# Kernel optimization log

Hardware: AMD Instinct MI355X
Metric: run time of the kernel (lower is better)

## Reference

```python
import jax, jax.numpy as jnp
import numpy as np

N, D, F, E, TOP_K = 8192, 1024, 2048, 8, 2


def setup_inputs() -> dict:
    key = jax.random.key(0)
    ks = jax.random.split(key, 8)
    s = 0.02
    x = jax.random.normal(ks[0], (N, D), dtype=jnp.float32)
    Wr = jax.random.normal(ks[1], (D, E), dtype=jnp.float32) * s  # router
    br = jnp.zeros((E,), jnp.float32)
    W1 = jax.random.normal(ks[2], (E, D, F), dtype=jnp.float32) * s  # expert FFN in
    b1 = jnp.zeros((E, F), jnp.float32)
    W2 = jax.random.normal(ks[3], (E, F, D), dtype=jnp.float32) * s  # expert FFN out
    b2 = jnp.zeros((E, D), jnp. float32)
    return {"x": x, "Wr": Wr, "br": br, "W1": W1, "b1": b1, "W2": W2, "b2": b2}


def reference(x, Wr, br, W1, b1, W2, b2):
    # Router: per-token expert logits -> softmax probabilities -> top-k sampler.
    logits = x @ Wr + br                         # [N, E]
    probs = jax.nn.softmax(logits, axis=-1)      # [N, E]
    top_p, top_i = jax.lax.top_k(probs, TOP_K)   # [N, K]
    # Combine weights: prob mass only on the selected top-k experts per token.
    w = (jax.nn.one_hot(top_i, E, dtype=x.dtype) * top_p[..., None]).sum(axis=1)  # [N, E]
    # Per-expert gather-compute-scatter, expressed as masked full-batch expert FFN
    # (identical math: tokens not routed to expert e have weight 0).
    out = jnp.zeros((x.shape[0], W2.shape[-1]), dtype=x.dtype)
    for e in range(E):  # small fixed loop over structurally distinct experts
        h = jax.nn.gelu(x @ W1[e] + b1[e])       # [N, F]
        y = h @ W2[e] + b2[e]                    # [N, D]
        out = out + w[:, e:e + 1] * y            # weighted scatter-add combine
    return out
```

## Files before the change

kernel.cpp:

```cpp
#include <hip/hip_runtime.h>
#include <hip/hip_bf16.h>


#define N_TOK 8192
#define DIM   1024
#define FF    2048
#define NE    8

typedef unsigned short ushort_t;
typedef __bf16 bf16x8 __attribute__((ext_vector_type(8)));
typedef float  f32x4  __attribute__((ext_vector_type(4)));
typedef unsigned short u16x8 __attribute__((ext_vector_type(8)));

__device__ __forceinline__ ushort_t f2bf(float f) {
    union { float f; unsigned int u; } v; v.f = f;
    unsigned int r = (v.u + 0x7FFFu + ((v.u >> 16) & 1u)) >> 16;
    return (ushort_t)r;
}

__device__ __forceinline__ void gload_lds16(const ushort_t* g, ushort_t* l) {
    __builtin_amdgcn_global_load_lds(
        (const __attribute__((address_space(1))) void*)g,
        (__attribute__((address_space(3))) void*)l,
        16, 0, 0);
}

__global__ __launch_bounds__(256) void transpose_conv_kernel(
    const float* __restrict__ in, ushort_t* __restrict__ out, int R, int C)
{
    __shared__ float tile[64][68];
    const int e = blockIdx.z;
    const float* I = in + (size_t)e * R * C;
    ushort_t*    O = out + (size_t)e * R * C;
    const int c0 = blockIdx.x * 64, r0 = blockIdx.y * 64;
    const int tid = threadIdx.x;
#pragma unroll
    for (int j = 0; j < 4; ++j) {
        int row = j * 16 + (tid >> 4);
        int col = (tid & 15) * 4;
        float4 v = *reinterpret_cast<const float4*>(&I[(size_t)(r0 + row) * C + c0 + col]);
        *reinterpret_cast<float4*>(&tile[row][col]) = v;
    }
    __syncthreads();
#pragma unroll
    for (int j = 0; j < 2; ++j) {
        int orow = j * 32 + (tid >> 3);
        int k0   = (tid & 7) * 8;
        u16x8 o;
#pragma unroll
        for (int k = 0; k < 8; ++k) o[k] = f2bf(tile[k0 + k][orow]);
        *reinterpret_cast<u16x8*>(&O[(size_t)(c0 + orow) * R + r0 + k0]) = o;
    }
}

__global__ __launch_bounds__(256) void router_kernel(
    const float* __restrict__ x, const float* __restrict__ Wr, const float* __restrict__ br,
    int* __restrict__ cnt, int* __restrict__ tok_list, float* __restrict__ w_list)
{
    __shared__ int   se0[64], se1[64];
    __shared__ float sw0[64], sw1[64];

    const int wid  = threadIdx.x >> 6;
    const int lane = threadIdx.x & 63;
    const int tblk = blockIdx.x * 64;

    for (int i = 0; i < 16; ++i) {
        const int li = wid * 16 + i;
        const int t  = tblk + li;
        const float* xr = x + (size_t)t * DIM;

        float acc[NE];
#pragma unroll
        for (int e = 0; e < NE; ++e) acc[e] = 0.f;
        for (int d = lane; d < DIM; d += 64) {
            float xv = xr[d];
            const float4* w4 = reinterpret_cast<const float4*>(Wr + (size_t)d * NE);
            float4 w0 = w4[0], w1 = w4[1];
            acc[0] += xv * w0.x; acc[1] += xv * w0.y; acc[2] += xv * w0.z; acc[3] += xv * w0.w;
            acc[4] += xv * w1.x; acc[5] += xv * w1.y; acc[6] += xv * w1.z; acc[7] += xv * w1.w;
        }
#pragma unroll
        for (int e = 0; e < NE; ++e) {
            for (int off = 32; off > 0; off >>= 1)
                acc[e] += __shfl_down(acc[e], off, 64);
        }
        if (lane == 0) {
            float l[NE];
#pragma unroll
            for (int e = 0; e < NE; ++e) l[e] = acc[e] + br[e];
            float mx = l[0];
#pragma unroll
            for (int e = 1; e < NE; ++e) mx = fmaxf(mx, l[e]);
            float p[NE], s = 0.f;
#pragma unroll
            for (int e = 0; e < NE; ++e) { p[e] = expf(l[e] - mx); s += p[e]; }
            float inv = 1.f / s;
            int e0 = 0;
#pragma unroll
            for (int e = 1; e < NE; ++e) if (l[e] > l[e0]) e0 = e;
            int e1 = (e0 == 0) ? 1 : 0;
#pragma unroll
            for (int e = 0; e < NE; ++e) if (e != e0 && l[e] > l[e1]) e1 = e;
            se0[li] = e0; sw0[li] = p[e0] * inv;
            se1[li] = e1; sw1[li] = p[e1] * inv;
        }
    }
    __syncthreads();

    if (threadIdx.x < 64) {
        const int t  = tblk + lane;
        const int e0 = se0[lane], e1 = se1[lane];
        const unsigned long long below = ((unsigned long long)1 << lane) - 1;
        int p0 = 0, p1 = 0;
#pragma unroll
        for (int e = 0; e < NE; ++e) {
            unsigned long long m0 = __ballot(e0 == e);
            unsigned long long m1 = __ballot(e1 == e);
            int c = __popcll(m0) + __popcll(m1);
            int b = 0;
            if (lane == e && c) b = atomicAdd(&cnt[e], c);
            b = __shfl(b, e, 64);
            if (e0 == e) p0 = b + __popcll(m0 & below);
            if (e1 == e) p1 = b + __popcll(m0) + __popcll(m1 & below);
        }
        tok_list[e0 * N_TOK + p0] = t;  w_list[e0 * N_TOK + p0] = sw0[lane];
        tok_list[e1 * N_TOK + p1] = t;  w_list[e1 * N_TOK + p1] = sw1[lane];
    }
}

__global__ void scan_kernel(const int* __restrict__ cnt, int* __restrict__ offs,
                            int* __restrict__ tile_e, int* __restrict__ tile_m0,
                            int* __restrict__ meta)
{
    if (threadIdx.x == 0 && blockIdx.x == 0) {
        int s = 0;
        for (int e = 0; e < NE; ++e) { offs[e] = s; s += cnt[e]; }
        offs[NE] = s;
        int nt = 0;
        for (int e = 0; e < NE; ++e)
            for (int m0 = 0; m0 < cnt[e]; m0 += 128) {
                tile_e[nt] = e; tile_m0[nt] = m0; ++nt;
            }
        meta[0] = nt;
    }
}

__global__ __launch_bounds__(256) void gather_a_kernel(
    const float* __restrict__ x, const int* __restrict__ offs,
    const int* __restrict__ tok_list, ushort_t* __restrict__ xpack)
{
    const int c   = blockIdx.x * 256 + threadIdx.x;
    const int row = c >> 7;
    int e = 0;
#pragma unroll
    for (int k = 1; k < NE; ++k) e += (row >= offs[k]);
    const int tok = tok_list[e * N_TOK + (row - offs[e])];
    const int d0  = (c & 127) << 3;
    const float* src = x + ((size_t)tok << 10) + d0;
    float4 a = *reinterpret_cast<const float4*>(src);
    float4 b = *reinterpret_cast<const float4*>(src + 4);
    u16x8 o;
    o[0] = f2bf(a.x); o[1] = f2bf(a.y); o[2] = f2bf(a.z); o[3] = f2bf(a.w);
    o[4] = f2bf(b.x); o[5] = f2bf(b.y); o[6] = f2bf(b.z); o[7] = f2bf(b.w);
    *reinterpret_cast<u16x8*>(xpack + ((size_t)row << 10) + d0) = o;
}

template <int MODE>
__global__ __launch_bounds__(256) void moe_gemm_kernel(
    const ushort_t* __restrict__ A,
    const ushort_t* __restrict__ Bt,
    const float*    __restrict__ bias,
    const int*      __restrict__ cnt,
    const int*      __restrict__ offs,
    const int*      __restrict__ tok_list,
    const float*    __restrict__ w_list,
    const int*      __restrict__ tile_e,
    const int*      __restrict__ tile_m0,
    const int*      __restrict__ meta,
    ushort_t*       __restrict__ hout,
    float*          __restrict__ out,
    int K, int NCOL)
{
    const int nmt = meta[0];
    const int NB  = NCOL >> 7;
    const int L   = nmt * NB;

    const int xcd = blockIdx.x & 7;
    const int q = L >> 3, r = L & 7;
    const int cstart = (xcd < r) ? xcd * (q + 1) : r * (q + 1) + (xcd - r) * q;
    const int clen   = (xcd < r) ? q + 1 : q;

    __shared__ ushort_t As[3][128 * 32];
    __shared__ ushort_t Bs[3][128 * 32];

    const int tid  = threadIdx.x;
    const int lane = tid & 63;
    const int wid  = tid >> 6;
    const int wr = (wid >> 1) * 64;
    const int wc = (wid & 1) * 64;
    const int la = lane & 15;
    const int kc = lane >> 4;

    for (int i = blockIdx.x >> 3; i < clen; i += 96) {
        const int tau = cstart + i;
        const int nb  = tau & (NB - 1);
        const int mt  = tau >> (NB == 16 ? 4 : 3);
        const int e   = tile_e[mt];
        const int m0  = tile_m0[mt];
        const int cnt_e  = cnt[e];
        const int offs_e = offs[e];
        const int n0  = nb * 128;

        __syncthreads();

        size_t asrc[2], bsrc[2];
#pragma unroll
        for (int j = 0; j < 2; ++j) {
            int c = tid + 256 * j;
            int row   = c >> 2;
            int chunk = (c & 3) ^ ((row >> 1) & 3);
            int entry = m0 + row;
            size_t arow;
            if (MODE == 0) {
                arow = (entry < cnt_e) ? (size_t)(offs_e + entry) * K : 0;
            } else {
                arow = (size_t)(offs_e + entry) * K;
            }
            asrc[j] = arow + (size_t)chunk * 8;
            int col = n0 + row;
            bsrc[j] = ((size_t)e * NCOL + col) * K + (size_t)chunk * 8;
        }

        f32x4 acc[4][4];
#pragma unroll
        for (int m = 0; m < 4; ++m)
#pragma unroll
            for (int n = 0; n < 4; ++n)
                acc[m][n] = (f32x4){0.f, 0.f, 0.f, 0.f};

        auto STAGE = [&](int t, int b) {
            int k0 = t * 32;
#pragma unroll
            for (int j = 0; j < 2; ++j) {
                gload_lds16(A  + asrc[j] + k0, &As[b][(tid + 256 * j) * 8]);
                gload_lds16(Bt + bsrc[j] + k0, &Bs[b][(tid + 256 * j) * 8]);
            }
        };

        auto COMPUTE = [&](int b) {
            bf16x8 af[4], bfr[4];
#pragma unroll
            for (int m = 0; m < 4; ++m) {
                int rr = wr + m * 16 + la;
                af[m] = *reinterpret_cast<const bf16x8*>(&As[b][(rr * 4 + (kc ^ ((rr >> 1) & 3))) * 8]);
            }
#pragma unroll
            for (int n = 0; n < 4; ++n) {
                int rr = wc + n * 16 + la;
                bfr[n] = *reinterpret_cast<const bf16x8*>(&Bs[b][(rr * 4 + (kc ^ ((rr >> 1) & 3))) * 8]);
            }
            __builtin_amdgcn_s_setprio(1);
#pragma unroll
            for (int m = 0; m < 4; ++m)
#pragma unroll
                for (int n = 0; n < 4; ++n)
                    acc[m][n] = __builtin_amdgcn_mfma_f32_16x16x32_bf16(af[m], bfr[n], acc[m][n], 0, 0, 0);
            __builtin_amdgcn_s_setprio(0);
        };

        const int nk = K / 32;
        STAGE(0, 0);
        STAGE(1, 1);
        for (int t = 0; t < nk - 1; ++t) {
            asm volatile("s_waitcnt vmcnt(4)" ::: "memory");
            __builtin_amdgcn_s_barrier();
            if (t + 2 < nk) STAGE(t + 2, (t + 2) % 3);
            COMPUTE(t % 3);
        }
        asm volatile("s_waitcnt vmcnt(0)" ::: "memory");
        __builtin_amdgcn_s_barrier();
        COMPUTE((nk - 1) % 3);

#pragma unroll
        for (int m = 0; m < 4; ++m) {
            int rbase = wr + m * 16 + (lane >> 4) * 4;
#pragma unroll
            for (int n = 0; n < 4; ++n) {
                int gcol = n0 + wc + n * 16 + la;
                float bi = bias[(size_t)e * NCOL + gcol];
#pragma unroll
                for (int jj = 0; jj < 4; ++jj) {
                    int entry = m0 + rbase + jj;
                    if (entry < cnt_e) {
                        float v = acc[m][n][jj] + bi;
                        if (MODE == 0) {
                            float u = 0.7978845608028654f * (v + 0.044715f * v * v * v);
                            float g = 0.5f * v * (1.f + tanhf(u));
                            hout[(size_t)(offs_e + entry) * NCOL + gcol] = f2bf(g);
                        } else {
                            int tok  = tok_list[e * N_TOK + entry];
                            float w  = w_list  [e * N_TOK + entry];
                            atomicAdd(&out[(size_t)tok * NCOL + gcol], w * v);
                        }
                    }
                }
            }
        }
    }
}

extern "C" void kernel_launch(void* const* d_in, const int* in_sizes, int n_in,
                              void* d_out, int out_size, void* d_ws, size_t ws_size,
                              hipStream_t stream)
{
    const float* x  = (const float*)d_in[0];
    const float* Wr = (const float*)d_in[1];
    const float* br = (const float*)d_in[2];
    const float* W1 = (const float*)d_in[3];
    const float* b1 = (const float*)d_in[4];
    const float* W2 = (const float*)d_in[5];
    const float* b2 = (const float*)d_in[6];
    float* out = (float*)d_out;

    char* ws = (char*)d_ws;
    size_t off = 0;
    auto alloc = [&](size_t bytes) -> void* {
        void* p = ws + off;
        off = (off + bytes + 255) & ~(size_t)255;
        return p;
    };
    ushort_t* w1t = (ushort_t*)alloc((size_t)NE * DIM * FF * 2);
    ushort_t* w2t = (ushort_t*)alloc((size_t)NE * DIM * FF * 2);
    ushort_t* xpack = (ushort_t*)alloc((size_t)2 * N_TOK * DIM * 2);
    ushort_t* h   = (ushort_t*)alloc(((size_t)2 * N_TOK + 256) * FF * 2);
    int*      cnt = (int*)alloc(NE * sizeof(int));
    int*      offs= (int*)alloc((NE + 1) * sizeof(int));
    int*   tok_list = (int*)alloc((size_t)NE * N_TOK * sizeof(int));
    float* w_list   = (float*)alloc((size_t)NE * N_TOK * sizeof(float));
    int*   tile_e   = (int*)alloc(256 * sizeof(int));
    int*   tile_m0  = (int*)alloc(256 * sizeof(int));
    int*   meta     = (int*)alloc(16 * sizeof(int));
    (void)ws_size; (void)in_sizes; (void)n_in;

    hipMemsetAsync(out, 0, (size_t)out_size * sizeof(float), stream);
    hipMemsetAsync(cnt, 0, NE * sizeof(int), stream);

    transpose_conv_kernel<<<dim3(FF / 64, DIM / 64, NE), 256, 0, stream>>>(W1, w1t, DIM, FF);
    transpose_conv_kernel<<<dim3(DIM / 64, FF / 64, NE), 256, 0, stream>>>(W2, w2t, FF, DIM);
    router_kernel<<<N_TOK / 64, 256, 0, stream>>>(x, Wr, br, cnt, tok_list, w_list);
    scan_kernel<<<1, 64, 0, stream>>>(cnt, offs, tile_e, tile_m0, meta);
    gather_a_kernel<<<(2 * N_TOK * DIM) / (8 * 256), 256, 0, stream>>>(x, offs, tok_list, xpack);

    moe_gemm_kernel<0><<<768, 256, 0, stream>>>(
        xpack, w1t, b1, cnt, offs, tok_list, w_list, tile_e, tile_m0, meta, h, nullptr, DIM, FF);
    moe_gemm_kernel<1><<<768, 256, 0, stream>>>(
        h, w2t, b2, cnt, offs, tok_list, w_list, tile_e, tile_m0, meta, nullptr, out, FF, DIM);
}
```

Baseline: 504.6 us.

## Fuse token gather into GEMM1, split-K GEMM2, and move to 512-thread blocks

Drops the separate gather kernel: x is converted to bf16 once in token order and the first GEMM loads rows indirectly through tok_list. Both GEMMs now use 512-thread blocks with 8 waves, each computing a 64x32 sub-tile, and one global-to-LDS load per thread per stage. The second GEMM splits K into two halves, adding bias only on the first half, so the tile count matches GEMM1 at the cost of doubling its atomic adds. GELU's tanh is rewritten in terms of exp2.

```diff
diff --git a/kernel.cpp b/kernel.cpp
--- a/kernel.cpp
+++ b/kernel.cpp
@@ -23,6 +23,18 @@
         (const __attribute__((address_space(1))) void*)g,
         (__attribute__((address_space(3))) void*)l,
         16, 0, 0);
+}
+
+__global__ __launch_bounds__(256) void convert_x_kernel(
+    const float* __restrict__ x, ushort_t* __restrict__ xb)
+{
+    size_t i = ((size_t)blockIdx.x * 256 + threadIdx.x) * 8;
+    float4 a = *reinterpret_cast<const float4*>(x + i);
+    float4 b = *reinterpret_cast<const float4*>(x + i + 4);
+    u16x8 o;
+    o[0] = f2bf(a.x); o[1] = f2bf(a.y); o[2] = f2bf(a.z); o[3] = f2bf(a.w);
+    o[4] = f2bf(b.x); o[5] = f2bf(b.y); o[6] = f2bf(b.z); o[7] = f2bf(b.w);
+    *reinterpret_cast<u16x8*>(xb + i) = o;
 }
 
 __global__ __launch_bounds__(256) void transpose_conv_kernel(
@@ -145,28 +157,8 @@
     }
 }
 
-__global__ __launch_bounds__(256) void gather_a_kernel(
-    const float* __restrict__ x, const int* __restrict__ offs,
-    const int* __restrict__ tok_list, ushort_t* __restrict__ xpack)
-{
-    const int c   = blockIdx.x * 256 + threadIdx.x;
-    const int row = c >> 7;
-    int e = 0;
-#pragma unroll
-    for (int k = 1; k < NE; ++k) e += (row >= offs[k]);
-    const int tok = tok_list[e * N_TOK + (row - offs[e])];
-    const int d0  = (c & 127) << 3;
-    const float* src = x + ((size_t)tok << 10) + d0;
-    float4 a = *reinterpret_cast<const float4*>(src);
-    float4 b = *reinterpret_cast<const float4*>(src + 4);
-    u16x8 o;
-    o[0] = f2bf(a.x); o[1] = f2bf(a.y); o[2] = f2bf(a.z); o[3] = f2bf(a.w);
-    o[4] = f2bf(b.x); o[5] = f2bf(b.y); o[6] = f2bf(b.z); o[7] = f2bf(b.w);
-    *reinterpret_cast<u16x8*>(xpack + ((size_t)row << 10) + d0) = o;
-}
-
 template <int MODE>
-__global__ __launch_bounds__(256) void moe_gemm_kernel(
+__global__ __launch_bounds__(512, 6) void moe_gemm_kernel(
     const ushort_t* __restrict__ A,
     const ushort_t* __restrict__ Bt,
     const float*    __restrict__ bias,
@@ -178,12 +170,13 @@
     const int*      __restrict__ tile_m0,
     const int*      __restrict__ meta,
     ushort_t*       __restrict__ hout,
-    float*          __restrict__ out,
-    int K, int NCOL)
-{
+    float*          __restrict__ out)
+{
+    const int K    = (MODE == 0) ? 1024 : 2048;
+    const int NCOL = (MODE == 0) ? 2048 : 1024;
+
     const int nmt = meta[0];
-    const int NB  = NCOL >> 7;
-    const int L   = nmt * NB;
+    const int L   = nmt << 4;
 
     const int xcd = blockIdx.x & 7;
     const int q = L >> 3, r = L & 7;
@@ -196,66 +189,62 @@
     const int tid  = threadIdx.x;
     const int lane = tid & 63;
     const int wid  = tid >> 6;
-    const int wr = (wid >> 1) * 64;
-    const int wc = (wid & 1) * 64;
+    const int wr = (wid >> 2) * 64;
+    const int wc = (wid & 3) * 32;
     const int la = lane & 15;
     const int kc = lane >> 4;
 
     for (int i = blockIdx.x >> 3; i < clen; i += 96) {
         const int tau = cstart + i;
-        const int nb  = tau & (NB - 1);
-        const int mt  = tau >> (NB == 16 ? 4 : 3);
+        const int mt  = tau >> 4;
+        int nb, kh;
+        if (MODE == 0) { nb = tau & 15; kh = 0; }
+        else           { kh = tau & 1;  nb = (tau >> 1) & 7; }
         const int e   = tile_e[mt];
         const int m0  = tile_m0[mt];
         const int cnt_e  = cnt[e];
         const int offs_e = offs[e];
         const int n0  = nb * 128;
+        const int koff = kh << 10;
 
         __syncthreads();
 
-        size_t asrc[2], bsrc[2];
-#pragma unroll
-        for (int j = 0; j < 2; ++j) {
-            int c = tid + 256 * j;
-            int row   = c >> 2;
-            int chunk = (c & 3) ^ ((row >> 1) & 3);
-            int entry = m0 + row;
-            size_t arow;
+        const int srow  = tid >> 2;
+        const int chunk = (tid & 3) ^ ((srow >> 1) & 3);
+        size_t asrc, bsrc;
+        {
+            int entry = m0 + srow;
             if (MODE == 0) {
-                arow = (entry < cnt_e) ? (size_t)(offs_e + entry) * K : 0;
+                int tok = (entry < cnt_e) ? tok_list[e * N_TOK + entry] : 0;
+                asrc = (size_t)tok * K + chunk * 8;
             } else {
-                arow = (size_t)(offs_e + entry) * K;
-            }
-            asrc[j] = arow + (size_t)chunk * 8;
-            int col = n0 + row;
-            bsrc[j] = ((size_t)e * NCOL + col) * K + (size_t)chunk * 8;
-        }
-
-        f32x4 acc[4][4];
+                asrc = (size_t)(offs_e + entry) * K + koff + chunk * 8;
+            }
+            bsrc = ((size_t)e * NCOL + n0 + srow) * K + koff + chunk * 8;
+        }
+
+        f32x4 acc[4][2];
 #pragma unroll
         for (int m = 0; m < 4; ++m)
 #pragma unroll
-            for (int n = 0; n < 4; ++n)
+            for (int n = 0; n < 2; ++n)
                 acc[m][n] = (f32x4){0.f, 0.f, 0.f, 0.f};
 
         auto STAGE = [&](int t, int b) {
             int k0 = t * 32;
-#pragma unroll
-            for (int j = 0; j < 2; ++j) {
-                gload_lds16(A  + asrc[j] + k0, &As[b][(tid + 256 * j) * 8]);
-                gload_lds16(Bt + bsrc[j] + k0, &Bs[b][(tid + 256 * j) * 8]);
-            }
+            gload_lds16(A  + asrc + k0, &As[b][tid * 8]);
+            gload_lds16(Bt + bsrc + k0, &Bs[b][tid * 8]);
         };
 
         auto COMPUTE = [&](int b) {
-            bf16x8 af[4], bfr[4];
+            bf16x8 af[4], bfr[2];
 #pragma unroll
             for (int m = 0; m < 4; ++m) {
                 int rr = wr + m * 16 + la;
                 af[m] = *reinterpret_cast<const bf16x8*>(&As[b][(rr * 4 + (kc ^ ((rr >> 1) & 3))) * 8]);
             }
 #pragma unroll
-            for (int n = 0; n < 4; ++n) {
+            for (int n = 0; n < 2; ++n) {
                 int rr = wc + n * 16 + la;
                 bfr[n] = *reinterpret_cast<const bf16x8*>(&Bs[b][(rr * 4 + (kc ^ ((rr >> 1) & 3))) * 8]);
             }
@@ -263,16 +252,16 @@
 #pragma unroll
             for (int m = 0; m < 4; ++m)
 #pragma unroll
-                for (int n = 0; n < 4; ++n)
+                for (int n = 0; n < 2; ++n)
                     acc[m][n] = __builtin_amdgcn_mfma_f32_16x16x32_bf16(af[m], bfr[n], acc[m][n], 0, 0, 0);
             __builtin_amdgcn_s_setprio(0);
         };
 
-        const int nk = K / 32;
+        const int nk = 32;
         STAGE(0, 0);
         STAGE(1, 1);
         for (int t = 0; t < nk - 1; ++t) {
-            asm volatile("s_waitcnt vmcnt(4)" ::: "memory");
+            asm volatile("s_waitcnt vmcnt(2)" ::: "memory");
             __builtin_amdgcn_s_barrier();
             if (t + 2 < nk) STAGE(t + 2, (t + 2) % 3);
             COMPUTE(t % 3);
@@ -285,9 +274,9 @@
         for (int m = 0; m < 4; ++m) {
             int rbase = wr + m * 16 + (lane >> 4) * 4;
 #pragma unroll
-            for (int n = 0; n < 4; ++n) {
+            for (int n = 0; n < 2; ++n) {
                 int gcol = n0 + wc + n * 16 + la;
-                float bi = bias[(size_t)e * NCOL + gcol];
+                float bi = (MODE == 1 && kh != 0) ? 0.f : bias[(size_t)e * NCOL + gcol];
 #pragma unroll
                 for (int jj = 0; jj < 4; ++jj) {
                     int entry = m0 + rbase + jj;
@@ -295,12 +284,13 @@
                         float v = acc[m][n][jj] + bi;
                         if (MODE == 0) {
                             float u = 0.7978845608028654f * (v + 0.044715f * v * v * v);
-                            float g = 0.5f * v * (1.f + tanhf(u));
-                            hout[(size_t)(offs_e + entry) * NCOL + gcol] = f2bf(g);
+                            float t2 = __builtin_amdgcn_exp2f(2.8853900817779268f * u);
+                            float g = v * (t2 / (t2 + 1.f));
+                            hout[(size_t)(offs_e + entry) * FF + gcol] = f2bf(g);
                         } else {
                             int tok  = tok_list[e * N_TOK + entry];
                             float w  = w_list  [e * N_TOK + entry];
-                            atomicAdd(&out[(size_t)tok * NCOL + gcol], w * v);
+                            atomicAdd(&out[(size_t)tok * DIM + gcol], w * v);
                         }
                     }
                 }
@@ -331,8 +321,8 @@
     };
     ushort_t* w1t = (ushort_t*)alloc((size_t)NE * DIM * FF * 2);
     ushort_t* w2t = (ushort_t*)alloc((size_t)NE * DIM * FF * 2);
-    ushort_t* xpack = (ushort_t*)alloc((size_t)2 * N_TOK * DIM * 2);
-    ushort_t* h   = (ushort_t*)alloc(((size_t)2 * N_TOK + 256) * FF * 2);
+    ushort_t* xb  = (ushort_t*)alloc((size_t)N_TOK * DIM * 2);
+    ushort_t* h   = (ushort_t*)alloc(((size_t)2 * N_TOK + 128) * FF * 2);
     int*      cnt = (int*)alloc(NE * sizeof(int));
     int*      offs= (int*)alloc((NE + 1) * sizeof(int));
     int*   tok_list = (int*)alloc((size_t)NE * N_TOK * sizeof(int));
@@ -345,14 +335,14 @@
     hipMemsetAsync(out, 0, (size_t)out_size * sizeof(float), stream);
     hipMemsetAsync(cnt, 0, NE * sizeof(int), stream);
 
+    convert_x_kernel<<<(N_TOK * DIM) / (8 * 256), 256, 0, stream>>>(x, xb);
     transpose_conv_kernel<<<dim3(FF / 64, DIM / 64, NE), 256, 0, stream>>>(W1, w1t, DIM, FF);
     transpose_conv_kernel<<<dim3(DIM / 64, FF / 64, NE), 256, 0, stream>>>(W2, w2t, FF, DIM);
     router_kernel<<<N_TOK / 64, 256, 0, stream>>>(x, Wr, br, cnt, tok_list, w_list);
     scan_kernel<<<1, 64, 0, stream>>>(cnt, offs, tile_e, tile_m0, meta);
-    gather_a_kernel<<<(2 * N_TOK * DIM) / (8 * 256), 256, 0, stream>>>(x, offs, tok_list, xpack);
-
-    moe_gemm_kernel<0><<<768, 256, 0, stream>>>(
-        xpack, w1t, b1, cnt, offs, tok_list, w_list, tile_e, tile_m0, meta, h, nullptr, DIM, FF);
-    moe_gemm_kernel<1><<<768, 256, 0, stream>>>(
-        h, w2t, b2, cnt, offs, tok_list, w_list, tile_e, tile_m0, meta, nullptr, out, FF, DIM);
-}
+
+    moe_gemm_kernel<0><<<768, 512, 0, stream>>>(
+        xb, w1t, b1, cnt, offs, tok_list, w_list, tile_e, tile_m0, meta, h, nullptr);
+    moe_gemm_kernel<1><<<768, 512, 0, stream>>>(
+        h, w2t, b2, cnt, offs, tok_list, w_list, tile_e, tile_m0, meta, nullptr, out);
+}
```

Result: faster. 453.9 us (-10.0%).
